# Kernel tuning notes

Hardware: AMD Instinct MI355X
Metric: run time of the kernel (lower is better)

The kernel has to match this reference:

```python
import jax, jax.numpy as jnp
import numpy as np

UP = 2
KSIZE = 3
RES = 64
LRELU_SLOPE = 0.2
ACT_GAIN = float(np.sqrt(2.0))  # def_gain of 'lrelu' in bias_act


def _setup_filter():
    # upfirdn2d.setup_filter([1,3,3,1]): normalize, make separable 2D filter
    f = jnp.array([1.0, 3.0, 3.0, 1.0], dtype=jnp.float32)
    f = f / jnp.sum(f)
    return jnp.outer(f, f)  # [4,4]


def _upfirdn2d_up2(x, f2):
    # Zero-insertion upsample by 2 + pad + FIR filter, gain = up**2.
    # Torch path: zero-insert to 2H, pad (3,2), conv 4-tap -> 2H+2.
    # lhs_dilation gives 2H-1; absorbing the trailing inserted zero into the
    # right pad ((3,3) instead of (3,2)) is exactly equivalent.
    B, C, H, W = x.shape
    k = (f2 * (UP * UP)).astype(x.dtype)[None, None]  # [1,1,4,4] (symmetric, flip-invariant)
    k = jnp.tile(k, (C, 1, 1, 1))                     # depthwise [C,1,4,4]
    return jax.lax.conv_general_dilated(
        x, k, window_strides=(1, 1), padding=((3, 3), (3, 3)),
        lhs_dilation=(UP, UP),
        dimension_numbers=('NCHW', 'OIHW', 'NCHW'),
        feature_group_count=C)


def setup_inputs() -> dict:
    key = jax.random.key(0)
    ks = jax.random.split(key, 6)
    B, Cin, Cout, Wd = 16, 512, 512, 512
    Hin = RES // UP
    return {
        "x": jax.random.normal(ks[0], (B, Cin, Hin, Hin), jnp.float32),
        "w": jax.random.normal(ks[1], (B, Wd), jnp.float32),
        "affine_weight": jax.random.normal(ks[2], (Cin, Wd), jnp.float32),
        "affine_bias": jnp.ones((Cin,), jnp.float32),  # bias_init=1
        "weight": jax.random.normal(ks[3], (Cout, Cin, KSIZE, KSIZE), jnp.float32),
        "bias": jnp.zeros((Cout,), jnp.float32),
        "noise_const": jax.random.normal(ks[4], (RES, RES), jnp.float32),
        "noise_strength": jax.random.uniform(ks[5], (), jnp.float32),
    }


def reference(x, w, affine_weight, affine_bias, weight, bias, noise_const, noise_strength):
    B, Cin, Hin, Win = x.shape
    Cout = weight.shape[0]
    # affine: FullyConnectedLayer, weight_gain = 1/sqrt(w_dim), bias_init=1
    styles = w @ affine_weight.T * (1.0 / np.sqrt(w.shape[1])) + affine_bias  # [B,Cin]
    # modulate + demodulate (fused_modconv=True): per-sample weights
    wmod = weight[None] * styles[:, None, :, None, None]                     # [B,Cout,Cin,kh,kw]
    dcoef = jax.lax.rsqrt(jnp.sum(jnp.square(wmod), axis=(2, 3, 4)) + 1e-8)  # [B,Cout]
    wmod = wmod * dcoef[:, :, None, None, None]
    # up=2 -> flip_weight=False -> true convolution: flip spatial taps
    wmod = wmod[..., ::-1, ::-1]
    # conv2d_resample: upfirdn2d upsample first (pad = k//2 + (fw+up-1)//2 = 3), then VALID conv
    xu = _upfirdn2d_up2(x, _setup_filter())                                  # [B,Cin,66,66]
    xr = xu.reshape(1, B * Cin, xu.shape[2], xu.shape[3])
    wr = wmod.reshape(B * Cout, Cin, KSIZE, KSIZE)
    y = jax.lax.conv_general_dilated(
        xr, wr, window_strides=(1, 1), padding='VALID',
        dimension_numbers=('NCHW', 'OIHW', 'NCHW'),
        feature_group_count=B)
    y = y.reshape(B, Cout, RES, RES)
    # noise_mode='const': noise = noise_const * noise_strength
    y = y + noise_const * noise_strength
    # fused bias + lrelu + def_gain (gain=1, conv_clamp=None)
    y = jax.nn.leaky_relu(y + bias[None, :, None, None], LRELU_SLOPE) * ACT_GAIN
    return y
```

## Files before the change

### kernel.cpp

```cpp
#include <hip/hip_runtime.h>
#include <hip/hip_bf16.h>
#include <math.h>

#define CIN   512
#define COUT  512
#define NB    16
#define WD    512
#define HIN   32
#define HUP   66
#define RES   64
#define LRELU 0.2f
#define ACT_GAIN 1.4142135623730951f

typedef __attribute__((ext_vector_type(8))) short short8;
typedef __attribute__((ext_vector_type(4))) float float4v;

__global__ void styles2_kernel(const float* __restrict__ w,
                               const float* __restrict__ aw,
                               const float* __restrict__ ab,
                               float* __restrict__ styles) {
    int b = blockIdx.x;
    int cig = blockIdx.y;
    int lane = threadIdx.x & 63, wv = threadIdx.x >> 6;
    __shared__ float wsh[WD];
    for (int e = threadIdx.x; e < WD; e += 256) wsh[e] = w[b * WD + e];
    __syncthreads();
    for (int r = 0; r < 16; ++r) {
        int ci = cig * 64 + wv * 16 + r;
        const float* arow = aw + (size_t)ci * WD;
        float acc = 0.f;
        for (int k = lane; k < WD; k += 64) acc += arow[k] * wsh[k];
        for (int off = 32; off; off >>= 1) acc += __shfl_down(acc, off, 64);
        if (lane == 0)
            styles[b * CIN + ci] = acc * 0.04419417382415922f + ab[ci];
    }
}

__global__ void prep_weights(const float* __restrict__ weight,
                             float* __restrict__ wsq,
                             __hip_bfloat16* __restrict__ wb) {
    int idx = blockIdx.x * 256 + threadIdx.x;
    int co = idx & (COUT - 1);
    int ci = idx >> 9;
    const float* wp = weight + ((size_t)co * CIN + ci) * 9;
    int cc = ci >> 5, chi = (ci >> 3) & 3, clo = ci & 7;
    float s = 0.f;
#pragma unroll
    for (int t = 0; t < 9; ++t) {
        float v = wp[t];
        s += v * v;
        int tf = 8 - t;
        wb[((((size_t)cc * 9 + tf) * 4 + chi) * COUT + co) * 8 + clo] = __float2bfloat16(v);
    }
    wsq[(size_t)co * CIN + ci] = s;
}

__global__ void dcoef2_kernel(const float* __restrict__ styles,
                              const float* __restrict__ wsq,
                              float* __restrict__ dcoef) {
    int b = blockIdx.x;
    int cog = blockIdx.y;
    int lane = threadIdx.x & 63, wv = threadIdx.x >> 6;
    __shared__ float s2[CIN];
    for (int e = threadIdx.x; e < CIN; e += 256) {
        float s = styles[b * CIN + e];
        s2[e] = s * s;
    }
    __syncthreads();
    for (int r = 0; r < 16; ++r) {
        int co = cog * 64 + wv * 16 + r;
        const float* qrow = wsq + (size_t)co * CIN;
        float acc = 0.f;
        for (int k = lane; k < CIN; k += 64) acc += qrow[k] * s2[k];
        for (int off = 32; off; off >>= 1) acc += __shfl_down(acc, off, 64);
        if (lane == 0) dcoef[b * COUT + co] = rsqrtf(acc + 1e-8f);
    }
}

__global__ void upmod2_kernel(const float* __restrict__ x,
                              const float* __restrict__ styles,
                              __hip_bfloat16* __restrict__ xs2) {
    __shared__ float xt[128 * 65];
    const int oh = blockIdx.x;
    const int ci0 = blockIdx.y * 128;
    const int b = blockIdx.z;
    int m0, m1; float a0, a1;
    if (oh & 1) { m0 = (oh - 3) >> 1; a0 = 0.125f; m1 = (oh - 1) >> 1; a1 = 0.375f; }
    else        { m0 = (oh >> 1) - 1; a0 = 0.375f; m1 = (oh >> 1);     a1 = 0.125f; }
    for (int e = threadIdx.x; e < 8192; e += 256) {
        int ci = e >> 6, sel = (e >> 5) & 1, iw = e & 31;
        int m = sel ? m1 : m0;
        float v = 0.f;
        if (m >= 0 && m < HIN)
            v = x[((size_t)(b * CIN + ci0 + ci) * HIN + m) * HIN + iw];
        xt[ci * 65 + sel * 32 + iw] = v;
    }
    __syncthreads();
    for (int e = threadIdx.x; e < 66 * 128; e += 256) {
        int ci = e & 127, ow = e >> 7;
        int n0i, n1i; float b0, b1;
        if (ow & 1) { n0i = (ow - 3) >> 1; b0 = 0.125f; n1i = (ow - 1) >> 1; b1 = 0.375f; }
        else        { n0i = (ow >> 1) - 1; b0 = 0.375f; n1i = (ow >> 1);     b1 = 0.125f; }
        bool c0 = (n0i >= 0) & (n0i < HIN);
        bool c1 = (n1i >= 0) & (n1i < HIN);
        float r0 = (c0 ? xt[ci * 65 + n0i] : 0.f) * b0 + (c1 ? xt[ci * 65 + n1i] : 0.f) * b1;
        float r1 = (c0 ? xt[ci * 65 + 32 + n0i] : 0.f) * b0 + (c1 ? xt[ci * 65 + 32 + n1i] : 0.f) * b1;
        float s = styles[b * CIN + ci0 + ci] * 4.0f;
        float val = (a0 * r0 + a1 * r1) * s;
        xs2[(((size_t)b * HUP + oh) * HUP + ow) * CIN + ci0 + ci] = __float2bfloat16(val);
    }
}

#define LDA_SZ 25600
#define LDB_SZ 36864

__global__ __launch_bounds__(256, 2) void conv_mfma(
        const __hip_bfloat16* __restrict__ xs2,
        const __hip_bfloat16* __restrict__ wb,
        const float* __restrict__ dcoef,
        const float* __restrict__ bias,
        const float* __restrict__ noise,
        const float* __restrict__ nstr,
        float* __restrict__ out)
{
    __shared__ __align__(16) char smem[LDA_SZ + LDB_SZ];
    const int tid = threadIdx.x;
    const int lane = tid & 63;
    const int wid = tid >> 6;
    const int li = lane & 15;
    const int q = lane >> 4;
    const int mt = blockIdx.x;
    const int n0 = blockIdx.y * 64;
    const int b  = blockIdx.z;
    const int y0 = mt * 4;

    long a_goff[7];
    int  a_lds[7];
#pragma unroll
    for (int k = 0; k < 7; ++k) {
        int n = wid + k * 4;
        if (n < 25) {
            int s = n * 64 + lane;
            if (s > 1583) s = 1583;
            int r = s / 264;
            int rem = s - r * 264;
            int chi = rem / 66;
            int col = rem - chi * 66;
            a_goff[k] = ((long)(b * HUP + y0 + r) * HUP + col) * CIN + chi * 8;
            a_lds[k] = n * 1024;
        } else { a_goff[k] = 0; a_lds[k] = -1; }
    }
    long b_goff[9];
#pragma unroll
    for (int k = 0; k < 9; ++k) {
        int sl = wid + k * 4;
        b_goff[k] = ((long)sl * COUT + n0) * 8 + (long)lane * 8;
    }

    float4v acc[4][4];
#pragma unroll
    for (int i = 0; i < 4; ++i)
#pragma unroll
        for (int j = 0; j < 4; ++j) acc[i][j] = (float4v)0.f;

    const char* xg = (const char*)xs2;
    const char* wg = (const char*)wb;

    for (int cc = 0; cc < 16; ++cc) {
#pragma unroll
        for (int k = 0; k < 9; ++k) {
            int sl = wid + k * 4;
            long ge = (long)cc * 147456 + b_goff[k];
            __builtin_amdgcn_global_load_lds(
                (const __attribute__((address_space(1))) char*)(wg + ge * 2),
                (__attribute__((address_space(3))) char*)(smem + LDA_SZ + sl * 1024),
                16, 0, 0);
        }
#pragma unroll
        for (int k = 0; k < 7; ++k) {
            if (a_lds[k] >= 0) {
                long ge = a_goff[k] + (long)cc * 32;
                __builtin_amdgcn_global_load_lds(
                    (const __attribute__((address_space(1))) char*)(xg + ge * 2),
                    (__attribute__((address_space(3))) char*)(smem + a_lds[k]),
                    16, 0, 0);
            }
        }
        __syncthreads();

#pragma unroll
        for (int t = 0; t < 9; ++t) {
            const int kh = t / 3, kw = t - kh * 3;
            short8 bf[4];
#pragma unroll
            for (int j = 0; j < 4; ++j)
                bf[j] = *(const short8*)(smem + LDA_SZ +
                        (((t * 4 + q) * 64) + j * 16 + li) * 16);
#pragma unroll
            for (int i = 0; i < 4; ++i) {
                short8 af = *(const short8*)(smem +
                        ((((wid + kh) * 4 + q) * 66) + (i * 16 + li + kw)) * 16);
#pragma unroll
                for (int j = 0; j < 4; ++j)
                    acc[i][j] = __builtin_amdgcn_mfma_f32_16x16x32_bf16(
                        af, bf[j], acc[i][j], 0, 0, 0);
            }
        }
        __syncthreads();
    }

    const float ns = nstr[0];
    const int row = y0 + wid;
#pragma unroll
    for (int j = 0; j < 4; ++j) {
        int cout = n0 + j * 16 + li;
        float dc = dcoef[b * COUT + cout];
        float bs = bias[cout];
        float* op = out + ((size_t)(b * COUT + cout) * RES + row) * RES;
#pragma unroll
        for (int i = 0; i < 4; ++i) {
            int colb = i * 16 + q * 4;
            float4v nz = *(const float4v*)(noise + row * RES + colb);
            float4v a = acc[i][j];
            float4v r;
            r.x = a.x * dc + nz.x * ns + bs;
            r.y = a.y * dc + nz.y * ns + bs;
            r.z = a.z * dc + nz.z * ns + bs;
            r.w = a.w * dc + nz.w * ns + bs;
            r.x = (r.x > 0.f ? r.x : LRELU * r.x) * ACT_GAIN;
            r.y = (r.y > 0.f ? r.y : LRELU * r.y) * ACT_GAIN;
            r.z = (r.z > 0.f ? r.z : LRELU * r.z) * ACT_GAIN;
            r.w = (r.w > 0.f ? r.w : LRELU * r.w) * ACT_GAIN;
            *(float4v*)(op + colb) = r;
        }
    }
}

extern "C" void kernel_launch(void* const* d_in, const int* in_sizes, int n_in,
                              void* d_out, int out_size, void* d_ws, size_t ws_size,
                              hipStream_t stream) {
    (void)in_sizes; (void)n_in; (void)out_size; (void)ws_size;
    const float* x     = (const float*)d_in[0];
    const float* w     = (const float*)d_in[1];
    const float* aw    = (const float*)d_in[2];
    const float* ab    = (const float*)d_in[3];
    const float* wt    = (const float*)d_in[4];
    const float* bias  = (const float*)d_in[5];
    const float* noise = (const float*)d_in[6];
    const float* nstr  = (const float*)d_in[7];
    float* out = (float*)d_out;

    char* ws = (char*)d_ws;
    float* styles = (float*)ws;
    float* dcoef  = (float*)(ws + 32768);
    float* wsq    = (float*)(ws + 65536);
    __hip_bfloat16* wb  = (__hip_bfloat16*)(ws + 65536 + 1048576);
    __hip_bfloat16* xs2 = (__hip_bfloat16*)(ws + 65536 + 1048576 + 4718592);

    styles2_kernel<<<dim3(NB, 8), dim3(256), 0, stream>>>(w, aw, ab, styles);
    prep_weights<<<dim3(1024), dim3(256), 0, stream>>>(wt, wsq, wb);
    dcoef2_kernel<<<dim3(NB, 8), dim3(256), 0, stream>>>(styles, wsq, dcoef);
    upmod2_kernel<<<dim3(HUP, 4, NB), dim3(256), 0, stream>>>(x, styles, xs2);
    conv_mfma<<<dim3(16, 8, NB), dim3(256), 0, stream>>>(
        xs2, wb, dcoef, bias, noise, nstr, out);
}
```

Baseline: 547.9 us.

## Double conv M-tile to 8 rows, rework upsample kernel and weight prep indexing

```diff
diff --git a/kernel.cpp b/kernel.cpp
--- a/kernel.cpp
+++ b/kernel.cpp
@@ -13,6 +13,7 @@
 #define ACT_GAIN 1.4142135623730951f
 
 typedef __attribute__((ext_vector_type(8))) short short8;
+typedef __attribute__((ext_vector_type(8))) unsigned short ushort8;
 typedef __attribute__((ext_vector_type(4))) float float4v;
 
 __global__ void styles2_kernel(const float* __restrict__ w,
@@ -40,8 +41,8 @@
                              float* __restrict__ wsq,
                              __hip_bfloat16* __restrict__ wb) {
     int idx = blockIdx.x * 256 + threadIdx.x;
-    int co = idx & (COUT - 1);
-    int ci = idx >> 9;
+    int ci = idx & (CIN - 1);
+    int co = idx >> 9;
     const float* wp = weight + ((size_t)co * CIN + ci) * 9;
     int cc = ci >> 5, chi = (ci >> 3) & 3, clo = ci & 7;
     float s = 0.f;
@@ -77,42 +78,96 @@
     }
 }
 
-__global__ void upmod2_kernel(const float* __restrict__ x,
-                              const float* __restrict__ styles,
-                              __hip_bfloat16* __restrict__ xs2) {
-    __shared__ float xt[128 * 65];
+__global__ __launch_bounds__(256) void upmod3_kernel(
+        const float* __restrict__ x,
+        const float* __restrict__ styles,
+        __hip_bfloat16* __restrict__ xs2) {
+    __shared__ __hip_bfloat16 xin[2][128][32];
+    __shared__ __align__(16) __hip_bfloat16 tt[66][136];
     const int oh = blockIdx.x;
-    const int ci0 = blockIdx.y * 128;
-    const int b = blockIdx.z;
+    const int b  = blockIdx.y;
+    const int tid = threadIdx.x;
+    const int lane = tid & 63;
+    const int wid = tid >> 6;
+
     int m0, m1; float a0, a1;
     if (oh & 1) { m0 = (oh - 3) >> 1; a0 = 0.125f; m1 = (oh - 1) >> 1; a1 = 0.375f; }
     else        { m0 = (oh >> 1) - 1; a0 = 0.375f; m1 = (oh >> 1);     a1 = 0.125f; }
-    for (int e = threadIdx.x; e < 8192; e += 256) {
-        int ci = e >> 6, sel = (e >> 5) & 1, iw = e & 31;
-        int m = sel ? m1 : m0;
-        float v = 0.f;
-        if (m >= 0 && m < HIN)
-            v = x[((size_t)(b * CIN + ci0 + ci) * HIN + m) * HIN + iw];
-        xt[ci * 65 + sel * 32 + iw] = v;
-    }
-    __syncthreads();
-    for (int e = threadIdx.x; e < 66 * 128; e += 256) {
-        int ci = e & 127, ow = e >> 7;
-        int n0i, n1i; float b0, b1;
-        if (ow & 1) { n0i = (ow - 3) >> 1; b0 = 0.125f; n1i = (ow - 1) >> 1; b1 = 0.375f; }
-        else        { n0i = (ow >> 1) - 1; b0 = 0.375f; n1i = (ow >> 1);     b1 = 0.125f; }
-        bool c0 = (n0i >= 0) & (n0i < HIN);
-        bool c1 = (n1i >= 0) & (n1i < HIN);
-        float r0 = (c0 ? xt[ci * 65 + n0i] : 0.f) * b0 + (c1 ? xt[ci * 65 + n1i] : 0.f) * b1;
-        float r1 = (c0 ? xt[ci * 65 + 32 + n0i] : 0.f) * b0 + (c1 ? xt[ci * 65 + 32 + n1i] : 0.f) * b1;
-        float s = styles[b * CIN + ci0 + ci] * 4.0f;
-        float val = (a0 * r0 + a1 * r1) * s;
-        xs2[(((size_t)b * HUP + oh) * HUP + ow) * CIN + ci0 + ci] = __float2bfloat16(val);
-    }
-}
-
-#define LDA_SZ 25600
-#define LDB_SZ 36864
+    const bool v0 = (m0 >= 0) & (m0 < HIN);
+    const bool v1 = (m1 >= 0) & (m1 < HIN);
+
+    int p0, p1, t0, t1; float w0c, w1c, u0c, u1c;
+    {
+        int ow = lane;
+        if (ow & 1) { p0 = (ow - 3) >> 1; w0c = 0.125f; p1 = (ow - 1) >> 1; w1c = 0.375f; }
+        else        { p0 = (ow >> 1) - 1; w0c = 0.375f; p1 = (ow >> 1);     w1c = 0.125f; }
+        if (p0 < 0 || p0 >= HIN) { p0 = 0; w0c = 0.f; }
+        if (p1 < 0 || p1 >= HIN) { p1 = 0; w1c = 0.f; }
+        int owt = 64 + (tid & 1);
+        if (owt & 1) { t0 = (owt - 3) >> 1; u0c = 0.125f; t1 = (owt - 1) >> 1; u1c = 0.375f; }
+        else         { t0 = (owt >> 1) - 1; u0c = 0.375f; t1 = (owt >> 1);     u1c = 0.125f; }
+        if (t0 < 0 || t0 >= HIN) { t0 = 0; u0c = 0.f; }
+        if (t1 < 0 || t1 >= HIN) { t1 = 0; u1c = 0.f; }
+    }
+    const int ow_t = 64 + (tid & 1);
+    const int ci_t = tid >> 1;
+
+    for (int ch = 0; ch < 4; ++ch) {
+        const int ci0c = ch * 128;
+#pragma unroll
+        for (int j = 0; j < 8; ++j) {
+            int e = tid + 256 * j;
+            int sel = e >> 10;
+            int ci = (e >> 3) & 127;
+            int f4 = e & 7;
+            int m = sel ? m1 : m0;
+            bool vv = sel ? v1 : v0;
+            float4 xv = make_float4(0.f, 0.f, 0.f, 0.f);
+            if (vv)
+                xv = *(const float4*)(x + (((size_t)(b * CIN + ci0c + ci)) * HIN + m) * HIN + f4 * 4);
+            __hip_bfloat16* d = &xin[sel][ci][f4 * 4];
+            d[0] = __float2bfloat16(xv.x);
+            d[1] = __float2bfloat16(xv.y);
+            d[2] = __float2bfloat16(xv.z);
+            d[3] = __float2bfloat16(xv.w);
+        }
+        __syncthreads();
+#pragma unroll 4
+        for (int k = 0; k < 32; ++k) {
+            int ci = wid * 32 + k;
+            float s = styles[b * CIN + ci0c + ci] * 4.0f;
+            float r0 = __bfloat162float(xin[0][ci][p0]) * w0c +
+                       __bfloat162float(xin[0][ci][p1]) * w1c;
+            float r1 = __bfloat162float(xin[1][ci][p0]) * w0c +
+                       __bfloat162float(xin[1][ci][p1]) * w1c;
+            tt[lane][ci] = __float2bfloat16((a0 * r0 + a1 * r1) * s);
+        }
+        {
+            float s = styles[b * CIN + ci0c + ci_t] * 4.0f;
+            float r0 = __bfloat162float(xin[0][ci_t][t0]) * u0c +
+                       __bfloat162float(xin[0][ci_t][t1]) * u1c;
+            float r1 = __bfloat162float(xin[1][ci_t][t0]) * u0c +
+                       __bfloat162float(xin[1][ci_t][t1]) * u1c;
+            tt[ow_t][ci_t] = __float2bfloat16((a0 * r0 + a1 * r1) * s);
+        }
+        __syncthreads();
+#pragma unroll
+        for (int j = 0; j < 5; ++j) {
+            int e = tid + 256 * j;
+            if (e < 1056) {
+                int ow = e >> 4, c8 = e & 15;
+                ushort8 v = *(const ushort8*)&tt[ow][c8 * 8];
+                *(ushort8*)(xs2 + (((size_t)b * HUP + oh) * HUP + ow) * CIN + ci0c + c8 * 8) = v;
+            }
+        }
+        __syncthreads();
+    }
+}
+
+#define A_SLICES 42
+#define A_BYTES  43008
+#define TOT_SLICES 78
+#define CONV_LDS (A_BYTES + 36864)
 
 __global__ __launch_bounds__(256, 2) void conv_mfma(
         const __hip_bfloat16* __restrict__ xs2,
@@ -123,7 +178,7 @@
         const float* __restrict__ nstr,
         float* __restrict__ out)
 {
-    __shared__ __align__(16) char smem[LDA_SZ + LDB_SZ];
+    extern __shared__ __align__(16) char smem[];
     const int tid = threadIdx.x;
     const int lane = tid & 63;
     const int wid = tid >> 6;
@@ -132,58 +187,48 @@
     const int mt = blockIdx.x;
     const int n0 = blockIdx.y * 64;
     const int b  = blockIdx.z;
-    const int y0 = mt * 4;
-
-    long a_goff[7];
-    int  a_lds[7];
-#pragma unroll
-    for (int k = 0; k < 7; ++k) {
-        int n = wid + k * 4;
-        if (n < 25) {
-            int s = n * 64 + lane;
-            if (s > 1583) s = 1583;
-            int r = s / 264;
-            int rem = s - r * 264;
-            int chi = rem / 66;
-            int col = rem - chi * 66;
-            a_goff[k] = ((long)(b * HUP + y0 + r) * HUP + col) * CIN + chi * 8;
-            a_lds[k] = n * 1024;
-        } else { a_goff[k] = 0; a_lds[k] = -1; }
-    }
-    long b_goff[9];
-#pragma unroll
-    for (int k = 0; k < 9; ++k) {
-        int sl = wid + k * 4;
-        b_goff[k] = ((long)sl * COUT + n0) * 8 + (long)lane * 8;
-    }
-
-    float4v acc[4][4];
-#pragma unroll
-    for (int i = 0; i < 4; ++i)
+    const int y0 = mt * 8;
+
+    const char* ga[20];
+    int lofs[20];
+#pragma unroll
+    for (int k = 0; k < 20; ++k) {
+        int sl = wid + 4 * k;
+        lofs[k] = sl * 1024;
+        if (sl < A_SLICES) {
+            int slot = sl * 64 + lane;
+            if (slot > 2639) slot = 2639;
+            int col = slot % 66;
+            int rem = slot / 66;
+            int chi = rem & 3;
+            int r = rem >> 2;
+            long elem = ((long)(b * HUP + y0 + r) * HUP + col) * CIN + chi * 8;
+            ga[k] = (const char*)xs2 + elem * 2;
+        } else if (sl < TOT_SLICES) {
+            int sb = sl - A_SLICES;
+            long elem = ((long)sb * COUT + n0 + lane) * 8;
+            ga[k] = (const char*)wb + elem * 2;
+        } else {
+            ga[k] = nullptr;
+        }
+    }
+
+    float4v acc[8][4];
+#pragma unroll
+    for (int i = 0; i < 8; ++i)
 #pragma unroll
         for (int j = 0; j < 4; ++j) acc[i][j] = (float4v)0.f;
 
-    const char* xg = (const char*)xs2;
-    const char* wg = (const char*)wb;
-
+#pragma unroll 1
     for (int cc = 0; cc < 16; ++cc) {
 #pragma unroll
-        for (int k = 0; k < 9; ++k) {
-            int sl = wid + k * 4;
-            long ge = (long)cc * 147456 + b_goff[k];
-            __builtin_amdgcn_global_load_lds(
-                (const __attribute__((address_space(1))) char*)(wg + ge * 2),
-                (__attribute__((address_space(3))) char*)(smem + LDA_SZ + sl * 1024),
-                16, 0, 0);
-        }
-#pragma unroll
-        for (int k = 0; k < 7; ++k) {
-            if (a_lds[k] >= 0) {
-                long ge = a_goff[k] + (long)cc * 32;
+        for (int k = 0; k < 20; ++k) {
+            if (ga[k]) {
                 __builtin_amdgcn_global_load_lds(
-                    (const __attribute__((address_space(1))) char*)(xg + ge * 2),
-                    (__attribute__((address_space(3))) char*)(smem + a_lds[k]),
+                    (const __attribute__((address_space(1))) char*)ga[k],
+                    (__attribute__((address_space(3))) char*)(smem + lofs[k]),
                     16, 0, 0);
+                ga[k] += (lofs[k] < A_BYTES) ? 64 : 294912;
             }
         }
         __syncthreads();
@@ -194,12 +239,13 @@
             short8 bf[4];
 #pragma unroll
             for (int j = 0; j < 4; ++j)
-                bf[j] = *(const short8*)(smem + LDA_SZ +
+                bf[j] = *(const short8*)(smem + A_BYTES +
                         (((t * 4 + q) * 64) + j * 16 + li) * 16);
 #pragma unroll
-            for (int i = 0; i < 4; ++i) {
+            for (int i = 0; i < 8; ++i) {
                 short8 af = *(const short8*)(smem +
-                        ((((wid + kh) * 4 + q) * 66) + (i * 16 + li + kw)) * 16);
+                        ((((2 * wid + (i >> 2) + kh) * 4 + q) * 66) +
+                         ((i & 3) * 16 + li + kw)) * 16);
 #pragma unroll
                 for (int j = 0; j < 4; ++j)
                     acc[i][j] = __builtin_amdgcn_mfma_f32_16x16x32_bf16(
@@ -210,28 +256,32 @@
     }
 
     const float ns = nstr[0];
-    const int row = y0 + wid;
+    float dc[4], bs[4];
 #pragma unroll
     for (int j = 0; j < 4; ++j) {
         int cout = n0 + j * 16 + li;
-        float dc = dcoef[b * COUT + cout];
-        float bs = bias[cout];
-        float* op = out + ((size_t)(b * COUT + cout) * RES + row) * RES;
-#pragma unroll
-        for (int i = 0; i < 4; ++i) {
-            int colb = i * 16 + q * 4;
-            float4v nz = *(const float4v*)(noise + row * RES + colb);
+        dc[j] = dcoef[b * COUT + cout];
+        bs[j] = bias[cout];
+    }
+#pragma unroll
+    for (int i = 0; i < 8; ++i) {
+        const int row = y0 + 2 * wid + (i >> 2);
+        const int colb = (i & 3) * 16 + q * 4;
+        float4v nz = *(const float4v*)(noise + row * RES + colb);
+#pragma unroll
+        for (int j = 0; j < 4; ++j) {
+            int cout = n0 + j * 16 + li;
             float4v a = acc[i][j];
             float4v r;
-            r.x = a.x * dc + nz.x * ns + bs;
-            r.y = a.y * dc + nz.y * ns + bs;
-            r.z = a.z * dc + nz.z * ns + bs;
-            r.w = a.w * dc + nz.w * ns + bs;
+            r.x = a.x * dc[j] + nz.x * ns + bs[j];
+            r.y = a.y * dc[j] + nz.y * ns + bs[j];
+            r.z = a.z * dc[j] + nz.z * ns + bs[j];
+            r.w = a.w * dc[j] + nz.w * ns + bs[j];
             r.x = (r.x > 0.f ? r.x : LRELU * r.x) * ACT_GAIN;
             r.y = (r.y > 0.f ? r.y : LRELU * r.y) * ACT_GAIN;
             r.z = (r.z > 0.f ? r.z : LRELU * r.z) * ACT_GAIN;
             r.w = (r.w > 0.f ? r.w : LRELU * r.w) * ACT_GAIN;
-            *(float4v*)(op + colb) = r;
+            *(float4v*)(out + (((size_t)b * COUT + cout) * RES + row) * RES + colb) = r;
         }
     }
 }
@@ -260,7 +310,7 @@
     styles2_kernel<<<dim3(NB, 8), dim3(256), 0, stream>>>(w, aw, ab, styles);
     prep_weights<<<dim3(1024), dim3(256), 0, stream>>>(wt, wsq, wb);
     dcoef2_kernel<<<dim3(NB, 8), dim3(256), 0, stream>>>(styles, wsq, dcoef);
-    upmod2_kernel<<<dim3(HUP, 4, NB), dim3(256), 0, stream>>>(x, styles, xs2);
-    conv_mfma<<<dim3(16, 8, NB), dim3(256), 0, stream>>>(
+    upmod3_kernel<<<dim3(HUP, NB), dim3(256), 0, stream>>>(x, styles, xs2);
+    conv_mfma<<<dim3(8, 8, NB), dim3(256), CONV_LDS, stream>>>(
         xs2, wb, dcoef, bias, noise, nstr, out);
 }
```

Result: slower. 836.0 us (+52.6%).
